# Kernel optimization log

Hardware: AMD Instinct MI355X
Metric: run time of the kernel (lower is better)

Reference implementation:

```python
import jax, jax.numpy as jnp
import numpy as np

N = 50000
E = 800000
F_IN, H1, H2, C = 512, 256, 32, 16


def _glorot(key, shape):
    lim = float(np.sqrt(6.0 / (shape[0] + shape[1])))
    return jax.random.uniform(key, shape, jnp.float32, -lim, lim)


def setup_inputs() -> dict:
    key = jax.random.key(0)
    ks = jax.random.split(key, 8)
    x = jax.random.normal(ks[0], (N, F_IN), jnp.float32)
    edge_index = jax.random.randint(ks[1], (2, E), 0, N, jnp.int64)
    return {
        "x": x,
        "edge_index": edge_index,
        "W1": _glorot(ks[2], (F_IN, H1)), "b1": jnp.zeros((H1,), jnp.float32),
        "W2": _glorot(ks[3], (H1, H2)), "b2": jnp.zeros((H2,), jnp.float32),
        "W3": _glorot(ks[4], (H2, C)), "b3": jnp.zeros((C,), jnp.float32),
    }


def _gcn_norm(edge_index, n_nodes):
    # Add self-loops, compute symmetric normalization deg^-1/2[src]*deg^-1/2[dst]
    loop = jnp.arange(n_nodes, dtype=edge_index.dtype)
    src = jnp.concatenate([edge_index[0], loop])
    dst = jnp.concatenate([edge_index[1], loop])
    ones = jnp.ones(src.shape[0], jnp.float32)
    deg = jax.ops.segment_sum(ones, dst, num_segments=n_nodes)
    dinv = jnp.where(deg > 0, jax.lax.rsqrt(deg), 0.0)
    norm = dinv[src] * dinv[dst]  # [E+N]
    return src, dst, norm


def _gcn_conv(x, W, b, src, dst, norm, n_nodes):
    h = x @ W  # transform first (reduces scatter width)
    msg = h[src] * norm[:, None]  # gather + scale, [E+N, out]
    out = jax.ops.segment_sum(msg, dst, num_segments=n_nodes)
    return out + b


def reference(x, edge_index, W1, b1, W2, b2, W3, b3):
    n_nodes = x.shape[0]
    src, dst, norm = _gcn_norm(edge_index, n_nodes)
    h = _gcn_conv(x, W1, b1, src, dst, norm, n_nodes)
    h = jax.nn.relu(h)  # dropout is identity in eval mode
    h = _gcn_conv(h, W2, b2, src, dst, norm, n_nodes)
    h = jax.nn.relu(h)
    h = _gcn_conv(h, W3, b3, src, dst, norm, n_nodes)
    return h
```

## Files before the change

### kernel.cpp

```cpp
#include <hip/hip_runtime.h>

constexpr int N   = 50000;
constexpr int E   = 800000;
constexpr int FIN = 512;
constexpr int H1v = 256;
constexpr int H2v = 32;
constexpr int Cv  = 16;

constexpr int NBLK = (N + 1023) / 1024;

typedef __attribute__((ext_vector_type(8))) short short8;
typedef __attribute__((ext_vector_type(4))) float f32x4;
typedef __attribute__((ext_vector_type(4))) unsigned short us4;
typedef __attribute__((ext_vector_type(4))) unsigned int uint4v;

__device__ inline unsigned short f2bf(float f) {
    unsigned u = __float_as_uint(f);
    return (unsigned short)((u + 0x7FFFu + ((u >> 16) & 1u)) >> 16);
}
__device__ inline float bf2f(unsigned short b) { return __uint_as_float(((unsigned)b) << 16); }


__global__ __launch_bounds__(256) void k_init(const float* __restrict__ W,
                                              unsigned short* __restrict__ Wf,
                                              int* __restrict__ cnt) {
    const int b = blockIdx.x;
    if (b < 64) {
        int t = b * 256 + threadIdx.x;
        int l = t & 63, nt = (t >> 6) & 15, kt = t >> 10;
        int n = nt * 16 + (l & 15);
        int kb = kt * 32 + (l >> 4) * 8;
        short8 h8, l8;
#pragma unroll
        for (int j = 0; j < 8; ++j) {
            float w = W[(size_t)(kb + j) * H1v + n];
            unsigned short h = f2bf(w);
            h8[j] = (short)h;
            l8[j] = (short)f2bf(w - bf2f(h));
        }
        size_t base = ((size_t)(kt * 16 + nt) * 2) * 512 + (size_t)l * 8;
        *(short8*)(Wf + base) = h8;
        *(short8*)(Wf + base + 512) = l8;
    } else {
        int i = (b - 64) * 256 + threadIdx.x;
        if (i <= N) cnt[i] = 0;
    }
}


__global__ __launch_bounds__(256) void k_hist(const int* __restrict__ dst,
                                              int* __restrict__ cnt) {
    int e = blockIdx.x * 256 + threadIdx.x;
    if (e < E) atomicAdd(&cnt[dst[e]], 1);
}

__global__ __launch_bounds__(256) void k_scan_part(const int* __restrict__ cnt,
                                                   int* __restrict__ bsum) {
    __shared__ int red[256];
    const int t = threadIdx.x;
    const int base = blockIdx.x * 1024 + t * 4;
    int s = 0;
#pragma unroll
    for (int i = 0; i < 4; ++i) {
        int idx = base + i;
        if (idx < N) s += cnt[idx];
    }
    red[t] = s;
    __syncthreads();
    for (int off = 128; off > 0; off >>= 1) {
        if (t < off) red[t] += red[t + off];
        __syncthreads();
    }
    if (t == 0) bsum[blockIdx.x] = red[0];
}

__global__ __launch_bounds__(256) void k_scan_final(const int* __restrict__ cnt,
                                                    const int* __restrict__ bsum,
                                                    int* __restrict__ row_ptr,
                                                    int* __restrict__ cursor,
                                                    float* __restrict__ dinv) {
    __shared__ int sums[256];
    __shared__ int s_bofs, s_tot;
    const int t = threadIdx.x;

    if (t < 64) {
        int v = (t < NBLK) ? bsum[t] : 0;
        int pre = (t < (int)blockIdx.x) ? v : 0;
#pragma unroll
        for (int off = 32; off > 0; off >>= 1) {
            pre += __shfl_down(pre, off, 64);
            v   += __shfl_down(v, off, 64);
        }
        if (t == 0) { s_bofs = pre; s_tot = v; }
    }

    const int base = blockIdx.x * 1024 + t * 4;
    int v[4];
    int local = 0;
#pragma unroll
    for (int i = 0; i < 4; ++i) {
        int idx = base + i;
        v[i] = (idx < N) ? cnt[idx] : 0;
        local += v[i];
    }
    sums[t] = local;
    __syncthreads();
    for (int off = 1; off < 256; off <<= 1) {
        int u = (t >= off) ? sums[t - off] : 0;
        __syncthreads();
        sums[t] += u;
        __syncthreads();
    }
    int run = s_bofs + sums[t] - local;
#pragma unroll
    for (int i = 0; i < 4; ++i) {
        int idx = base + i;
        if (idx < N) {
            row_ptr[idx] = run;
            cursor[idx] = run;
            dinv[idx] = rsqrtf(1.0f + (float)v[i]);
        }
        run += v[i];
    }
    if (blockIdx.x == NBLK - 1 && t == 0) row_ptr[N] = s_tot;
}

__global__ __launch_bounds__(256) void k_permute(const int* __restrict__ src,
                                                 const int* __restrict__ dst,
                                                 int* __restrict__ cursor,
                                                 int* __restrict__ srcs) {
    int e = blockIdx.x * 256 + threadIdx.x;
    if (e < E) {
        int pos = atomicAdd(&cursor[dst[e]], 1);
        srcs[pos] = src[e];
    }
}


__device__ inline void split_pair(float x0, float x1, unsigned& hp, unsigned& lp) {
    unsigned u0 = __float_as_uint(x0), u1 = __float_as_uint(x1);
    unsigned h0 = u0 & 0xffff0000u, h1 = u1 & 0xffff0000u;
    float l0 = x0 - __uint_as_float(h0);
    float l1 = x1 - __uint_as_float(h1);
    hp = __builtin_amdgcn_perm(u1, u0, 0x07060302u);
    lp = __builtin_amdgcn_perm(__float_as_uint(l1), __float_as_uint(l0), 0x07060302u);
}

__device__ inline void split_frag(const float4& a, const float4& b, short8& hi, short8& lo) {
    unsigned h0, h1, h2, h3, l0, l1, l2, l3;
    split_pair(a.x, a.y, h0, l0);
    split_pair(a.z, a.w, h1, l1);
    split_pair(b.x, b.y, h2, l2);
    split_pair(b.z, b.w, h3, l3);
    uint4v h, l;
    h[0] = h0; h[1] = h1; h[2] = h2; h[3] = h3;
    l[0] = l0; l[1] = l1; l[2] = l2; l[3] = l3;
    hi = __builtin_bit_cast(short8, h);
    lo = __builtin_bit_cast(short8, l);
}

__global__ __launch_bounds__(256, 2) void k_gemm1_mfma(const float* __restrict__ X,
                                                       const unsigned short* __restrict__ Wf,
                                                       const float* __restrict__ dinv,
                                                       unsigned short* __restrict__ Hout) {
    const int tid = threadIdx.x;
    const int w = tid >> 6, l = tid & 63;
    const int wr = w >> 1, wc = w & 1;
    const int row0 = blockIdx.x * 128 + wr * 64;
    const int colb = blockIdx.y;
    const int lm = l & 15;
    const int lk = (l >> 4) * 8;

    const float* ap[4];
    bool ok[4];
#pragma unroll
    for (int i = 0; i < 4; ++i) {
        int r = row0 + i * 16 + lm;
        ok[i] = r < N;
        ap[i] = X + (size_t)r * FIN + lk;
    }
    const unsigned short* bp0 = Wf + (size_t)(colb * 8 + wc * 4) * 1024 + (size_t)l * 8;

    f32x4 acc[4][4];
#pragma unroll
    for (int i = 0; i < 4; ++i)
#pragma unroll
        for (int j = 0; j < 4; ++j) acc[i][j] = (f32x4)0.f;

    float4 a0[4], a1[4];
#pragma unroll
    for (int i = 0; i < 4; ++i) {
        a0[i] = ok[i] ? *(const float4*)(ap[i]) : make_float4(0.f, 0.f, 0.f, 0.f);
        a1[i] = ok[i] ? *(const float4*)(ap[i] + 4) : make_float4(0.f, 0.f, 0.f, 0.f);
    }

    for (int ktg = 0; ktg < 16; ++ktg) {
        const unsigned short* bp = bp0 + (size_t)ktg * 16384;
        short8 Bh[4], Bl[4];
#pragma unroll
        for (int j = 0; j < 4; ++j) {
            Bh[j] = *(const short8*)(bp + j * 1024);
            Bl[j] = *(const short8*)(bp + j * 1024 + 512);
        }

        short8 Ah[4], Al[4];
#pragma unroll
        for (int i = 0; i < 4; ++i) split_frag(a0[i], a1[i], Ah[i], Al[i]);

        if (ktg < 15) {
#pragma unroll
            for (int i = 0; i < 4; ++i) {
                const float* p = ap[i] + (ktg + 1) * 32;
                a0[i] = ok[i] ? *(const float4*)(p) : make_float4(0.f, 0.f, 0.f, 0.f);
                a1[i] = ok[i] ? *(const float4*)(p + 4) : make_float4(0.f, 0.f, 0.f, 0.f);
            }
        }

#pragma unroll
        for (int i = 0; i < 4; ++i)
#pragma unroll
            for (int j = 0; j < 4; ++j) {
                acc[i][j] = __builtin_amdgcn_mfma_f32_16x16x32_bf16(Ah[i], Bh[j], acc[i][j], 0, 0, 0);
                acc[i][j] = __builtin_amdgcn_mfma_f32_16x16x32_bf16(Ah[i], Bl[j], acc[i][j], 0, 0, 0);
                acc[i][j] = __builtin_amdgcn_mfma_f32_16x16x32_bf16(Al[i], Bh[j], acc[i][j], 0, 0, 0);
            }
    }

    const int col0 = colb * 128;
#pragma unroll
    for (int i = 0; i < 4; ++i) {
        int rbase = row0 + i * 16 + (l >> 4) * 4;
        float dv[4];
        bool okr[4];
#pragma unroll
        for (int r = 0; r < 4; ++r) {
            int rr = rbase + r;
            okr[r] = rr < N;
            dv[r] = okr[r] ? dinv[rr] : 0.f;
        }
#pragma unroll
        for (int j = 0; j < 4; ++j) {
            int col = col0 + (wc * 4 + j) * 16 + lm;
#pragma unroll
            for (int r = 0; r < 4; ++r)
                if (okr[r]) Hout[(size_t)(rbase + r) * H1v + col] = f2bf(acc[i][j][r] * dv[r]);
        }
    }
}


__global__ __launch_bounds__(256) void k_gemm2(const float* __restrict__ A,
                                               const float* __restrict__ W,
                                               const float* __restrict__ dinv,
                                               unsigned short* __restrict__ Hout) {
    __shared__ float Ws[H1v * H2v];
    const int tid = threadIdx.x;
#pragma unroll
    for (int i = 0; i < 8; ++i) {
        int off = tid * 4 + i * 1024;
        *(float4*)(&Ws[off]) = *(const float4*)(W + off);
    }
    __syncthreads();

    const int row = blockIdx.x * 8 + (tid >> 5);
    const int col = tid & 31;
    if (row >= N) return;
    const float* arow = A + (size_t)row * H1v;
    float sum = 0.f;
#pragma unroll 4
    for (int k = 0; k < H1v; k += 4) {
        float4 a4 = *(const float4*)(arow + k);
        sum = fmaf(a4.x, Ws[(k + 0) * H2v + col], sum);
        sum = fmaf(a4.y, Ws[(k + 1) * H2v + col], sum);
        sum = fmaf(a4.z, Ws[(k + 2) * H2v + col], sum);
        sum = fmaf(a4.w, Ws[(k + 3) * H2v + col], sum);
    }
    Hout[(size_t)row * H2v + col] = f2bf(sum * dinv[row]);
}


__global__ __launch_bounds__(256) void k_agg_d256(const unsigned short* __restrict__ h,
                                                  const int* __restrict__ rp,
                                                  const int* __restrict__ srcs,
                                                  const float* __restrict__ dinv,
                                                  const float* __restrict__ bias,
                                                  float* __restrict__ out) {
    const int wave = threadIdx.x >> 6;
    const int lane = threadIdx.x & 63;
    const int d = blockIdx.x * 4 + wave;
    if (d >= N) return;
    const int beg = rp[d], end = rp[d + 1];
    const int fo = lane * 4;
    us4 sv = *(const us4*)(h + (size_t)d * H1v + fo);
    float ax = bf2f(sv.x), ay = bf2f(sv.y), az = bf2f(sv.z), aw = bf2f(sv.w);
    int j = beg;
    for (; j + 3 < end; j += 4) {
        int s0 = srcs[j], s1 = srcs[j + 1], s2 = srcs[j + 2], s3 = srcs[j + 3];
        us4 v0 = *(const us4*)(h + (size_t)s0 * H1v + fo);
        us4 v1 = *(const us4*)(h + (size_t)s1 * H1v + fo);
        us4 v2 = *(const us4*)(h + (size_t)s2 * H1v + fo);
        us4 v3 = *(const us4*)(h + (size_t)s3 * H1v + fo);
        ax += bf2f(v0.x) + bf2f(v1.x) + bf2f(v2.x) + bf2f(v3.x);
        ay += bf2f(v0.y) + bf2f(v1.y) + bf2f(v2.y) + bf2f(v3.y);
        az += bf2f(v0.z) + bf2f(v1.z) + bf2f(v2.z) + bf2f(v3.z);
        aw += bf2f(v0.w) + bf2f(v1.w) + bf2f(v2.w) + bf2f(v3.w);
    }
    for (; j < end; ++j) {
        us4 v = *(const us4*)(h + (size_t)srcs[j] * H1v + fo);
        ax += bf2f(v.x); ay += bf2f(v.y); az += bf2f(v.z); aw += bf2f(v.w);
    }
    const float di = dinv[d];
    const float4 b4 = *(const float4*)(bias + fo);
    float4 o;
    o.x = fmaxf(fmaf(di, ax, b4.x), 0.f);
    o.y = fmaxf(fmaf(di, ay, b4.y), 0.f);
    o.z = fmaxf(fmaf(di, az, b4.z), 0.f);
    o.w = fmaxf(fmaf(di, aw, b4.w), 0.f);
    *(float4*)(out + (size_t)d * H1v + fo) = o;
}


__global__ __launch_bounds__(256) void k_agg32_gemm3(const unsigned short* __restrict__ h2,
                                                     const int* __restrict__ rp,
                                                     const int* __restrict__ srcs,
                                                     const float* __restrict__ dinv,
                                                     const float* __restrict__ b2,
                                                     const float* __restrict__ W3,
                                                     unsigned short* __restrict__ h3) {
    __shared__ float als[8][33];
    __shared__ float W3s[H2v * Cv];
    const int t = threadIdx.x;
    *(float2*)(&W3s[t * 2]) = *(const float2*)(W3 + t * 2);

    const int sub = t >> 5, f = t & 31;
    const int d = blockIdx.x * 8 + sub;
    const int beg = rp[d], end = rp[d + 1];
    float acc = bf2f(h2[(size_t)d * H2v + f]);
    int j = beg;
    for (; j + 3 < end; j += 4) {
        float v0 = bf2f(h2[(size_t)srcs[j] * H2v + f]);
        float v1 = bf2f(h2[(size_t)srcs[j + 1] * H2v + f]);
        float v2 = bf2f(h2[(size_t)srcs[j + 2] * H2v + f]);
        float v3 = bf2f(h2[(size_t)srcs[j + 3] * H2v + f]);
        acc += v0 + v1 + v2 + v3;
    }
    for (; j < end; ++j) acc += bf2f(h2[(size_t)srcs[j] * H2v + f]);
    als[sub][f] = fmaxf(fmaf(dinv[d], acc, b2[f]), 0.f);
    __syncthreads();

    if (t < 128) {
        const int row = t >> 4, col = t & 15;
        float sum = 0.f;
#pragma unroll
        for (int k = 0; k < H2v; ++k) sum = fmaf(als[row][k], W3s[k * Cv + col], sum);
        const int gr = blockIdx.x * 8 + row;
        h3[(size_t)gr * Cv + col] = f2bf(sum * dinv[gr]);
    }
}


__global__ __launch_bounds__(256) void k_agg16(const unsigned short* __restrict__ h,
                                               const int* __restrict__ rp,
                                               const int* __restrict__ srcs,
                                               const float* __restrict__ dinv,
                                               const float* __restrict__ bias,
                                               float* __restrict__ out) {
    const int sub = threadIdx.x >> 4;
    const int f = threadIdx.x & 15;
    const int d = blockIdx.x * 16 + sub;
    if (d >= N) return;
    const int beg = rp[d], end = rp[d + 1];
    float acc = bf2f(h[(size_t)d * Cv + f]);
    int j = beg;
    for (; j + 3 < end; j += 4) {
        float v0 = bf2f(h[(size_t)srcs[j] * Cv + f]);
        float v1 = bf2f(h[(size_t)srcs[j + 1] * Cv + f]);
        float v2 = bf2f(h[(size_t)srcs[j + 2] * Cv + f]);
        float v3 = bf2f(h[(size_t)srcs[j + 3] * Cv + f]);
        acc += v0 + v1 + v2 + v3;
    }
    for (; j < end; ++j) acc += bf2f(h[(size_t)srcs[j] * Cv + f]);
    out[(size_t)d * Cv + f] = fmaf(dinv[d], acc, bias[f]);
}


extern "C" void kernel_launch(void* const* d_in, const int* in_sizes, int n_in,
                              void* d_out, int out_size, void* d_ws, size_t ws_size,
                              hipStream_t stream) {
    const float* x  = (const float*)d_in[0];
    const int*   ei = (const int*)d_in[1];
    const float* W1 = (const float*)d_in[2];
    const float* b1 = (const float*)d_in[3];
    const float* W2 = (const float*)d_in[4];
    const float* b2 = (const float*)d_in[5];
    const float* W3 = (const float*)d_in[6];
    const float* b3 = (const float*)d_in[7];
    const int* src = ei;
    const int* dst = ei + E;
    float* out = (float*)d_out;

    char* ws = (char*)d_ws;
    float* dinv   = (float*)ws;
    int*   cnt    = (int*)(ws + 0x40000);
    int*   rp     = cnt;
    int*   cursor = (int*)(ws + 0x80000);
    int*   bsum   = (int*)(ws + 0xB2000);
    int*   srcs   = (int*)(ws + 0xC0000);
    unsigned short* wsplit = (unsigned short*)(ws + (size_t)4 * 1024 * 1024);
    char* p = ws + (size_t)5 * 1024 * 1024;
    unsigned short* h1 = (unsigned short*)p; p += (size_t)N * H1v * sizeof(unsigned short);
    float*          a1 = (float*)p;          p += (size_t)N * H1v * sizeof(float);
    unsigned short* h2 = (unsigned short*)p; p += (size_t)N * H2v * sizeof(unsigned short);
    unsigned short* h3 = (unsigned short*)p;

    k_init<<<64 + (N + 256) / 256, 256, 0, stream>>>(W1, wsplit, cnt);
    k_hist<<<(E + 255) / 256, 256, 0, stream>>>(dst, cnt);
    k_scan_part<<<NBLK, 256, 0, stream>>>(cnt, bsum);
    k_scan_final<<<NBLK, 256, 0, stream>>>(cnt, bsum, rp, cursor, dinv);
    k_permute<<<(E + 255) / 256, 256, 0, stream>>>(src, dst, cursor, srcs);

    dim3 g1((N + 127) / 128, 2);
    k_gemm1_mfma<<<g1, 256, 0, stream>>>(x, wsplit, dinv, h1);
    k_agg_d256<<<(N + 3) / 4, 256, 0, stream>>>(h1, rp, srcs, dinv, b1, a1);

    k_gemm2<<<N / 8, 256, 0, stream>>>(a1, W2, dinv, h2);

    k_agg32_gemm3<<<N / 8, 256, 0, stream>>>(h2, rp, srcs, dinv, b2, W3, h3);

    k_agg16<<<(N + 15) / 16, 256, 0, stream>>>(h3, rp, srcs, dinv, b3, out);
}
```

Before: 465.9 us.

## Fuse layer-1 aggregation with layer-2 GEMM through shared memory

Merges the 256-wide neighbor aggregation and the 256x32 GEMM into one kernel. Aggregated rows stay in LDS and are multiplied against a transposed W2 that k_init prepares, so the fp32 a1 intermediate (about 51 MB written and read back) is never stored. The gather loop is also unrolled to 8 loads in flight. In exchange only half the threads do the GEMM phase and every block reads W2t from global or cache, which adds a block-wide sync and some idle lanes.

```diff
diff --git a/kernel.cpp b/kernel.cpp
--- a/kernel.cpp
+++ b/kernel.cpp
@@ -21,8 +21,10 @@
 __device__ inline float bf2f(unsigned short b) { return __uint_as_float(((unsigned)b) << 16); }
 
 
-__global__ __launch_bounds__(256) void k_init(const float* __restrict__ W,
+__global__ __launch_bounds__(256) void k_init(const float* __restrict__ W1,
+                                              const float* __restrict__ W2,
                                               unsigned short* __restrict__ Wf,
+                                              float* __restrict__ W2t,
                                               int* __restrict__ cnt) {
     const int b = blockIdx.x;
     if (b < 64) {
@@ -33,7 +35,7 @@
         short8 h8, l8;
 #pragma unroll
         for (int j = 0; j < 8; ++j) {
-            float w = W[(size_t)(kb + j) * H1v + n];
+            float w = W1[(size_t)(kb + j) * H1v + n];
             unsigned short h = f2bf(w);
             h8[j] = (short)h;
             l8[j] = (short)f2bf(w - bf2f(h));
@@ -41,8 +43,16 @@
         size_t base = ((size_t)(kt * 16 + nt) * 2) * 512 + (size_t)l * 8;
         *(short8*)(Wf + base) = h8;
         *(short8*)(Wf + base + 512) = l8;
+    } else if (b == 64) {
+        const int t = threadIdx.x;
+        const int col = t & 31, kb = t >> 5;
+#pragma unroll
+        for (int i = 0; i < 32; ++i) {
+            int k = i * 8 + kb;
+            W2t[col * H1v + k] = W2[k * H2v + col];
+        }
     } else {
-        int i = (b - 64) * 256 + threadIdx.x;
+        int i = (b - 65) * 256 + threadIdx.x;
         if (i <= N) cnt[i] = 0;
     }
 }
@@ -249,74 +259,62 @@
 }
 
 
-__global__ __launch_bounds__(256) void k_gemm2(const float* __restrict__ A,
-                                               const float* __restrict__ W,
-                                               const float* __restrict__ dinv,
-                                               unsigned short* __restrict__ Hout) {
-    __shared__ float Ws[H1v * H2v];
-    const int tid = threadIdx.x;
-#pragma unroll
-    for (int i = 0; i < 8; ++i) {
-        int off = tid * 4 + i * 1024;
-        *(float4*)(&Ws[off]) = *(const float4*)(W + off);
-    }
-    __syncthreads();
-
-    const int row = blockIdx.x * 8 + (tid >> 5);
-    const int col = tid & 31;
-    if (row >= N) return;
-    const float* arow = A + (size_t)row * H1v;
-    float sum = 0.f;
-#pragma unroll 4
-    for (int k = 0; k < H1v; k += 4) {
-        float4 a4 = *(const float4*)(arow + k);
-        sum = fmaf(a4.x, Ws[(k + 0) * H2v + col], sum);
-        sum = fmaf(a4.y, Ws[(k + 1) * H2v + col], sum);
-        sum = fmaf(a4.z, Ws[(k + 2) * H2v + col], sum);
-        sum = fmaf(a4.w, Ws[(k + 3) * H2v + col], sum);
-    }
-    Hout[(size_t)row * H2v + col] = f2bf(sum * dinv[row]);
-}
-
-
-__global__ __launch_bounds__(256) void k_agg_d256(const unsigned short* __restrict__ h,
-                                                  const int* __restrict__ rp,
-                                                  const int* __restrict__ srcs,
-                                                  const float* __restrict__ dinv,
-                                                  const float* __restrict__ bias,
-                                                  float* __restrict__ out) {
+__global__ __launch_bounds__(256) void k_agg256_gemm2(const unsigned short* __restrict__ h1,
+                                                      const int* __restrict__ rp,
+                                                      const int* __restrict__ srcs,
+                                                      const float* __restrict__ dinv,
+                                                      const float* __restrict__ b1,
+                                                      const float* __restrict__ W2t,
+                                                      unsigned short* __restrict__ h2) {
+    __shared__ float als[4][260];
     const int wave = threadIdx.x >> 6;
     const int lane = threadIdx.x & 63;
     const int d = blockIdx.x * 4 + wave;
-    if (d >= N) return;
     const int beg = rp[d], end = rp[d + 1];
     const int fo = lane * 4;
-    us4 sv = *(const us4*)(h + (size_t)d * H1v + fo);
+
+    us4 sv = *(const us4*)(h1 + (size_t)d * H1v + fo);
     float ax = bf2f(sv.x), ay = bf2f(sv.y), az = bf2f(sv.z), aw = bf2f(sv.w);
     int j = beg;
-    for (; j + 3 < end; j += 4) {
-        int s0 = srcs[j], s1 = srcs[j + 1], s2 = srcs[j + 2], s3 = srcs[j + 3];
-        us4 v0 = *(const us4*)(h + (size_t)s0 * H1v + fo);
-        us4 v1 = *(const us4*)(h + (size_t)s1 * H1v + fo);
-        us4 v2 = *(const us4*)(h + (size_t)s2 * H1v + fo);
-        us4 v3 = *(const us4*)(h + (size_t)s3 * H1v + fo);
-        ax += bf2f(v0.x) + bf2f(v1.x) + bf2f(v2.x) + bf2f(v3.x);
-        ay += bf2f(v0.y) + bf2f(v1.y) + bf2f(v2.y) + bf2f(v3.y);
-        az += bf2f(v0.z) + bf2f(v1.z) + bf2f(v2.z) + bf2f(v3.z);
-        aw += bf2f(v0.w) + bf2f(v1.w) + bf2f(v2.w) + bf2f(v3.w);
+    for (; j + 7 < end; j += 8) {
+        us4 v[8];
+#pragma unroll
+        for (int q = 0; q < 8; ++q)
+            v[q] = *(const us4*)(h1 + (size_t)srcs[j + q] * H1v + fo);
+#pragma unroll
+        for (int q = 0; q < 8; ++q) {
+            ax += bf2f(v[q].x); ay += bf2f(v[q].y);
+            az += bf2f(v[q].z); aw += bf2f(v[q].w);
+        }
     }
     for (; j < end; ++j) {
-        us4 v = *(const us4*)(h + (size_t)srcs[j] * H1v + fo);
+        us4 v = *(const us4*)(h1 + (size_t)srcs[j] * H1v + fo);
         ax += bf2f(v.x); ay += bf2f(v.y); az += bf2f(v.z); aw += bf2f(v.w);
     }
     const float di = dinv[d];
-    const float4 b4 = *(const float4*)(bias + fo);
-    float4 o;
-    o.x = fmaxf(fmaf(di, ax, b4.x), 0.f);
-    o.y = fmaxf(fmaf(di, ay, b4.y), 0.f);
-    o.z = fmaxf(fmaf(di, az, b4.z), 0.f);
-    o.w = fmaxf(fmaf(di, aw, b4.w), 0.f);
-    *(float4*)(out + (size_t)d * H1v + fo) = o;
+    const float4 b4 = *(const float4*)(b1 + fo);
+    als[wave][fo + 0] = fmaxf(fmaf(di, ax, b4.x), 0.f);
+    als[wave][fo + 1] = fmaxf(fmaf(di, ay, b4.y), 0.f);
+    als[wave][fo + 2] = fmaxf(fmaf(di, az, b4.z), 0.f);
+    als[wave][fo + 3] = fmaxf(fmaf(di, aw, b4.w), 0.f);
+    __syncthreads();
+
+    if (threadIdx.x < 128) {
+        const int row = threadIdx.x >> 5, col = threadIdx.x & 31;
+        const float* wcol = W2t + (size_t)col * H1v;
+        float sum = 0.f;
+#pragma unroll 8
+        for (int k = 0; k < H1v; k += 4) {
+            float4 wv = *(const float4*)(wcol + k);
+            float4 av = *(const float4*)(&als[row][k]);
+            sum = fmaf(av.x, wv.x, sum);
+            sum = fmaf(av.y, wv.y, sum);
+            sum = fmaf(av.z, wv.z, sum);
+            sum = fmaf(av.w, wv.w, sum);
+        }
+        const int gd = blockIdx.x * 4 + row;
+        h2[(size_t)gd * H2v + col] = f2bf(sum * dinv[gd]);
+    }
 }
 
 
@@ -406,14 +404,14 @@
     int*   cursor = (int*)(ws + 0x80000);
     int*   bsum   = (int*)(ws + 0xB2000);
     int*   srcs   = (int*)(ws + 0xC0000);
-    unsigned short* wsplit = (unsigned short*)(ws + (size_t)4 * 1024 * 1024);
+    unsigned short* wsplit = (unsigned short*)(ws + 0x400000);
+    float* w2t    = (float*)(ws + 0x480000);
     char* p = ws + (size_t)5 * 1024 * 1024;
     unsigned short* h1 = (unsigned short*)p; p += (size_t)N * H1v * sizeof(unsigned short);
-    float*          a1 = (float*)p;          p += (size_t)N * H1v * sizeof(float);
     unsigned short* h2 = (unsigned short*)p; p += (size_t)N * H2v * sizeof(unsigned short);
     unsigned short* h3 = (unsigned short*)p;
 
-    k_init<<<64 + (N + 256) / 256, 256, 0, stream>>>(W1, wsplit, cnt);
+    k_init<<<65 + (N + 256) / 256, 256, 0, stream>>>(W1, W2, wsplit, w2t, cnt);
     k_hist<<<(E + 255) / 256, 256, 0, stream>>>(dst, cnt);
     k_scan_part<<<NBLK, 256, 0, stream>>>(cnt, bsum);
     k_scan_final<<<NBLK, 256, 0, stream>>>(cnt, bsum, rp, cursor, dinv);
@@ -421,9 +419,8 @@
 
     dim3 g1((N + 127) / 128, 2);
     k_gemm1_mfma<<<g1, 256, 0, stream>>>(x, wsplit, dinv, h1);
-    k_agg_d256<<<(N + 3) / 4, 256, 0, stream>>>(h1, rp, srcs, dinv, b1, a1);
-
-    k_gemm2<<<N / 8, 256, 0, stream>>>(a1, W2, dinv, h2);
+
+    k_agg256_gemm2<<<N / 4, 256, 0, stream>>>(h1, rp, srcs, dinv, b1, w2t, h2);
 
     k_agg32_gemm3<<<N / 8, 256, 0, stream>>>(h2, rp, srcs, dinv, b2, W3, h3);
 
```

Result: slower. 567.0 us (+21.7%).
